# Kernel optimization log

Measured on AMD Instinct MI355X. Metric: run time of the kernel, lower is better.

## Reference

```python
import jax, jax.numpy as jnp
import numpy as np

BATCH = 1024
INPUT_DIM = 4096
HV_DIM = 8192          # == 2**NUM_QUBITS, so encode_classical fully overwrites the state
NUM_QUBITS = 13
QUANTUM_DEPTH = 3


def setup_inputs() -> dict:
    key = jax.random.key(0)
    k1, k2, k3 = jax.random.split(key, 3)
    x = jax.random.normal(k1, (BATCH, INPUT_DIM), dtype=jnp.float32)
    # torch nn.Linear weight layout: [out_features, in_features]
    W = jax.random.normal(k2, (HV_DIM, INPUT_DIM), dtype=jnp.float32)
    quantum_params = jax.random.normal(k3, (QUANTUM_DEPTH, NUM_QUBITS), dtype=jnp.float32)
    return {"x": x, "W": W, "quantum_params": quantum_params}


def reference(x, W, quantum_params):
    # projection: classical_hv = x @ W^T  -> [B, HV_DIM]
    classical = x @ W.T
    # encode_classical: normalize, cast to complex, renormalize (second norm is 1;
    # kept for fidelity with the original code path)
    amps = (classical / jnp.linalg.norm(classical, axis=-1, keepdims=True)).astype(jnp.complex64)
    amps = amps / jnp.linalg.norm(amps, axis=-1, keepdims=True)

    # sequential gate sequence: for depth in range(D): for qubit in range(Q):
    #   amps = amps*cos(a/2) + roll(amps, 1)*sin(a/2)*1j
    # each step uses the updated amplitudes -> lax.scan over the flattened angles
    angles = quantum_params.reshape(-1)  # [D*Q], depth-major matching the loop order

    def step(a, angle):
        c = jnp.cos(angle * 0.5)
        s = jnp.sin(angle * 0.5)
        return a * c + jnp.roll(a, 1, axis=-1) * (s * 1j), None

    amps, _ = jax.lax.scan(step, amps, angles)
    return amps  # [B, 2**NUM_QUBITS] complex64 quantum amplitudes
```

## Files before the change

### kernel.cpp

```cpp
#include <hip/hip_runtime.h>
#include <hip/hip_fp16.h>
#include <math.h>

typedef _Float16 half8 __attribute__((ext_vector_type(8)));
typedef __fp16 fp16x2 __attribute__((ext_vector_type(2)));
typedef float f32x4 __attribute__((ext_vector_type(4)));

#define BATCH 1024
#define IN_DIM 4096
#define HV 8192
#define NTAP 40

#define BM 128
#define BN 128
#define BK 32
#define BKP 36

#define BM2 128
#define BN2 256
#define BK2 64
#define NT2 (IN_DIM / BK2)
#define ASZ (BM2 * BK2)
#define BSZ (BN2 * BK2)
#define TSZ (ASZ + BSZ)

#define GLD16(g, l) __builtin_amdgcn_global_load_lds(                          \
    (const __attribute__((address_space(1))) void*)(g),                        \
    (__attribute__((address_space(3))) void*)(l), 16, 0, 0)

static __device__ __forceinline__ half8 pk8(f32x4 a, f32x4 b) {
    union { fp16x2 p[4]; half8 h; } u;
    u.p[0] = __builtin_amdgcn_cvt_pkrtz(a.x, a.y);
    u.p[1] = __builtin_amdgcn_cvt_pkrtz(a.z, a.w);
    u.p[2] = __builtin_amdgcn_cvt_pkrtz(b.x, b.y);
    u.p[3] = __builtin_amdgcn_cvt_pkrtz(b.z, b.w);
    return u.h;
}

typedef _Float16 half4v __attribute__((ext_vector_type(4)));
__global__ __launch_bounds__(256) void cvt_f32_f16(const float4* __restrict__ src,
                                                   half4v* __restrict__ dst, int n4) {
    int i = blockIdx.x * 256 + threadIdx.x;
    if (i < n4) {
        float4 v = src[i];
        half4v h;
        h.x = (_Float16)v.x; h.y = (_Float16)v.y;
        h.z = (_Float16)v.z; h.w = (_Float16)v.w;
        dst[i] = h;
    }
}

__global__ __launch_bounds__(64) void compute_taps(const float* __restrict__ qp,
                                                   float* __restrict__ taps) {
    const int lane = threadIdx.x;
    float qv = (lane < 39) ? qp[lane] : 0.f;
    float pr = (lane == 0) ? 1.f : 0.f;
    float pim = 0.f;
    for (int t = 0; t < 39; t++) {
        float a = __shfl(qv, t, 64) * 0.5f;
        float c = cosf(a), s = sinf(a);
        float ur = __shfl_up(pr, 1, 64);
        float ui = __shfl_up(pim, 1, 64);
        if (lane == 0) { ur = 0.f; ui = 0.f; }
        float nr = c * pr - s * ui;
        float ni = c * pim + s * ur;
        pr = nr; pim = ni;
    }
    if (lane < NTAP) taps[lane] = pr;
}

__global__ __launch_bounds__(512, 2) void gemm_f16(
        const _Float16* __restrict__ A,
        const _Float16* __restrict__ B,
        float* __restrict__ out,
        long out_n) {
    __shared__ __align__(16) _Float16 lds[3 * TSZ];

    const int tid  = threadIdx.x;
    const int lane = tid & 63;
    const int wave = tid >> 6;
    const int wm = wave & 1;
    const int wn = wave >> 1;
    const int q = lane >> 4, r = lane & 15;
    const int bm = blockIdx.y * BM2;
    const int bn = blockIdx.x * BN2;

    const _Float16* srcA[2];
    int dA[2];
    #pragma unroll
    for (int h = 0; h < 2; h++) {
        const int p = h * 512 + tid;
        const int R = p >> 3, c = (p & 7) ^ (R & 7);
        srcA[h] = A + (size_t)(bm + R) * IN_DIM + c * 8;
        dA[h] = (h * 512 + wave * 64) * 8;
    }
    const _Float16* srcB[4];
    int dB[4];
    #pragma unroll
    for (int h = 0; h < 4; h++) {
        const int p = h * 512 + tid;
        const int R = p >> 3, c = (p & 7) ^ (R & 7);
        srcB[h] = B + (size_t)(bn + R) * IN_DIM + c * 8;
        dB[h] = ASZ + (h * 512 + wave * 64) * 8;
    }

    f32x4 acc[4][4] = {};

#define STAGE(u, k0)  do {                                   \
        _Float16* bp = &lds[(u) * TSZ];                      \
        GLD16(srcA[0] + (k0), bp + dA[0]);                   \
        GLD16(srcA[1] + (k0), bp + dA[1]);                   \
        GLD16(srcB[0] + (k0), bp + dB[0]);                   \
        GLD16(srcB[1] + (k0), bp + dB[1]);                   \
        GLD16(srcB[2] + (k0), bp + dB[2]);                   \
        GLD16(srcB[3] + (k0), bp + dB[3]);                   \
    } while (0)

#define COMPUTE(u)  do {                                                            \
        const _Float16* bp = &lds[(u) * TSZ];                                       \
        half8 af[4][2], bf[4][2];                                                   \
        _Pragma("unroll")                                                           \
        for (int i = 0; i < 4; i++)                                                 \
            _Pragma("unroll")                                                       \
            for (int kk = 0; kk < 2; kk++) {                                        \
                const int R = wm * 64 + i * 16 + r;                                 \
                const int sw = (kk * 4 + q) ^ (r & 7);                              \
                af[i][kk] = *(const half8*)&bp[R * 64 + sw * 8];                    \
            }                                                                       \
        _Pragma("unroll")                                                           \
        for (int j = 0; j < 4; j++)                                                 \
            _Pragma("unroll")                                                       \
            for (int kk = 0; kk < 2; kk++) {                                        \
                const int R = wn * 64 + j * 16 + r;                                 \
                const int sw = (kk * 4 + q) ^ (r & 7);                              \
                bf[j][kk] = *(const half8*)&bp[ASZ + R * 64 + sw * 8];              \
            }                                                                       \
        __builtin_amdgcn_s_setprio(1);                                              \
        _Pragma("unroll")                                                           \
        for (int i = 0; i < 4; i++)                                                 \
            _Pragma("unroll")                                                       \
            for (int j = 0; j < 4; j++)                                             \
                _Pragma("unroll")                                                   \
                for (int kk = 0; kk < 2; kk++)                                      \
                    acc[i][j] = __builtin_amdgcn_mfma_f32_16x16x32_f16(             \
                        af[i][kk], bf[j][kk], acc[i][j], 0, 0, 0);                  \
        __builtin_amdgcn_s_setprio(0);                                              \
    } while (0)

    STAGE(0, 0);
    STAGE(1, BK2);
    int cur = 0;
    for (int t = 0; t < NT2 - 1; ++t) {
        asm volatile("s_waitcnt vmcnt(6)" ::: "memory");
        __builtin_amdgcn_sched_barrier(0);
        __builtin_amdgcn_s_barrier();
        if (t + 2 < NT2) {
            const int nxt = (cur + 2 >= 3) ? cur - 1 : cur + 2;
            STAGE(nxt, (t + 2) * BK2);
        }
        COMPUTE(cur);
        cur = (cur + 1 == 3) ? 0 : cur + 1;
    }
    asm volatile("s_waitcnt vmcnt(0)" ::: "memory");
    __builtin_amdgcn_sched_barrier(0);
    __builtin_amdgcn_s_barrier();
    COMPUTE(cur);
#undef STAGE
#undef COMPUTE

    #pragma unroll
    for (int i = 0; i < 4; i++) {
        const int row = bm + wm * 64 + i * 16 + q * 4;
        #pragma unroll
        for (int j = 0; j < 4; j++) {
            const int col = bn + wn * 64 + j * 16 + r;
            #pragma unroll
            for (int reg = 0; reg < 4; reg++) {
                long idx = (long)(row + reg) * HV + col;
                if (idx < out_n) out[idx] = acc[i][j][reg];
            }
        }
    }
}

__global__ __launch_bounds__(256) void gemm_f32in(
        const float* __restrict__ A, const float* __restrict__ B,
        float* __restrict__ out, long out_n) {
    __shared__ __align__(16) float lgA[BM * BKP];
    __shared__ __align__(16) float lgB[BN * BKP];

    const int tid  = threadIdx.x;
    const int lane = tid & 63;
    const int wave = tid >> 6;
    const int wm = wave & 1, wn = wave >> 1;
    const int q = lane >> 4, r = lane & 15;
    const int bm = blockIdx.y * BM;
    const int bn = blockIdx.x * BN;

    const int rg = lane >> 3;
    const int cg = (lane & 7) * 4;
    const float* gA = A + (size_t)(bm + wave * 32 + rg) * IN_DIM + cg;
    const float* gB = B + (size_t)(bn + wave * 32 + rg) * IN_DIM + cg;
    float* lA = &lgA[(wave * 32 + rg) * BKP + cg];
    float* lB = &lgB[(wave * 32 + rg) * BKP + cg];

    f32x4 acc[4][4] = {};

    for (int k0 = 0; k0 < IN_DIM; k0 += BK) {
        float4 va[4], vb[4];
        #pragma unroll
        for (int i = 0; i < 4; i++) {
            va[i] = *(const float4*)(gA + k0 + (size_t)(8 * i) * IN_DIM);
            vb[i] = *(const float4*)(gB + k0 + (size_t)(8 * i) * IN_DIM);
        }
        __syncthreads();
        #pragma unroll
        for (int i = 0; i < 4; i++) {
            *(float4*)(lA + 8 * i * BKP) = va[i];
            *(float4*)(lB + 8 * i * BKP) = vb[i];
        }
        __syncthreads();

        half8 af[4], bf[4];
        #pragma unroll
        for (int i = 0; i < 4; i++) {
            const float* p = &lgA[(wm * 64 + i * 16 + r) * BKP + q * 8];
            af[i] = pk8(*(const f32x4*)p, *(const f32x4*)(p + 4));
        }
        #pragma unroll
        for (int j = 0; j < 4; j++) {
            const float* p = &lgB[(wn * 64 + j * 16 + r) * BKP + q * 8];
            bf[j] = pk8(*(const f32x4*)p, *(const f32x4*)(p + 4));
        }

        #pragma unroll
        for (int i = 0; i < 4; i++)
            #pragma unroll
            for (int j = 0; j < 4; j++)
                acc[i][j] = __builtin_amdgcn_mfma_f32_16x16x32_f16(af[i], bf[j], acc[i][j], 0, 0, 0);
    }

    #pragma unroll
    for (int i = 0; i < 4; i++) {
        const int row = bm + wm * 64 + i * 16 + q * 4;
        #pragma unroll
        for (int j = 0; j < 4; j++) {
            const int col = bn + wn * 64 + j * 16 + r;
            #pragma unroll
            for (int reg = 0; reg < 4; reg++) {
                long idx = (long)(row + reg) * HV + col;
                if (idx < out_n) out[idx] = acc[i][j][reg];
            }
        }
    }
}

#define SW4(p4) ((p4) ^ (((p4) >> 3) & 7))
__global__ __launch_bounds__(256) void norm_conv(float* __restrict__ out,
                                                 const float* __restrict__ qp,
                                                 const float* __restrict__ taps,
                                                 long out_n) {
    __shared__ __align__(16) float ldsv[40 + HV + 24];
    __shared__ float scr[NTAP];
    __shared__ float red[4];

    const int b = blockIdx.x;
    if ((long)(b + 1) * HV > out_n) return;

    const int tid = threadIdx.x;
    const int lane = tid & 63;
    const int wave = tid >> 6;
    float* rowp = out + (size_t)b * HV;
    const float4* row4 = (const float4*)rowp;
    float4* l4 = (float4*)ldsv;

    float ss = 0.f;
    #pragma unroll
    for (int it = 0; it < 8; it++) {
        int j = it * 256 + tid;
        float4 v = row4[j];
        ss += v.x * v.x + v.y * v.y + v.z * v.z + v.w * v.w;
        l4[SW4(10 + j)] = v;
    }
    if (tid < NTAP) {
        ldsv[(SW4(tid >> 2) << 2) | (tid & 3)] = rowp[HV - NTAP + tid];
    }

    #pragma unroll
    for (int off = 32; off > 0; off >>= 1) ss += __shfl_down(ss, off, 64);
    if (lane == 0) red[wave] = ss;

    if (taps) {
        if (tid < NTAP) scr[tid] = taps[tid];
    } else if (wave == 0) {
        float qv = (lane < 39) ? qp[lane] : 0.f;
        float pr = (lane == 0) ? 1.f : 0.f;
        float pim = 0.f;
        for (int t = 0; t < 39; t++) {
            float a = __shfl(qv, t, 64) * 0.5f;
            float c = cosf(a), s = sinf(a);
            float ur = __shfl_up(pr, 1, 64);
            float ui = __shfl_up(pim, 1, 64);
            if (lane == 0) { ur = 0.f; ui = 0.f; }
            float nr = c * pr - s * ui;
            float ni = c * pim + s * ur;
            pr = nr; pim = ni;
        }
        if (lane < NTAP) scr[lane] = pr;
    }
    __syncthreads();

    const float inv = 1.0f / sqrtf(red[0] + red[1] + red[2] + red[3]);

    float w[72];
    #pragma unroll
    for (int t = 0; t < 18; t++) ((float4*)w)[t] = l4[SW4(8 * tid + t)];

    float4* out4 = (float4*)rowp;
    #pragma unroll
    for (int h = 0; h < 2; h++) {
        float av[16] = {};
        #pragma unroll
        for (int k = 0; k < NTAP; k++) {
            const float c = scr[k];
            #pragma unroll
            for (int o = 0; o < 16; o++) av[o] += c * w[40 + h * 16 + o - k];
        }
        #pragma unroll
        for (int t = 0; t < 4; t++) {
            out4[8 * tid + 4 * h + t] = make_float4(inv * av[4 * t], inv * av[4 * t + 1],
                                                    inv * av[4 * t + 2], inv * av[4 * t + 3]);
        }
    }
}

extern "C" void kernel_launch(void* const* d_in, const int* in_sizes, int n_in,
                              void* d_out, int out_size, void* d_ws, size_t ws_size,
                              hipStream_t stream) {
    const float* x  = (const float*)d_in[0];
    const float* W  = (const float*)d_in[1];
    const float* qp = (const float*)d_in[2];
    float* out = (float*)d_out;
    long out_n = (long)out_size;

    const size_t need = (size_t)BATCH * IN_DIM * 2 + (size_t)HV * IN_DIM * 2;

    if (ws_size >= need) {
        _Float16* xh = (_Float16*)d_ws;
        _Float16* wh = xh + (size_t)BATCH * IN_DIM;
        float* taps = nullptr;
        if (ws_size >= need + 256) {
            taps = (float*)((char*)d_ws + need);
            compute_taps<<<1, 64, 0, stream>>>(qp, taps);
        }
        int n4x = BATCH * IN_DIM / 4;
        int n4w = HV * IN_DIM / 4;
        cvt_f32_f16<<<n4x / 256, 256, 0, stream>>>((const float4*)x, (half4v*)xh, n4x);
        cvt_f32_f16<<<n4w / 256, 256, 0, stream>>>((const float4*)W, (half4v*)wh, n4w);
        dim3 grid2(HV / BN2, BATCH / BM2);
        gemm_f16<<<grid2, 512, 0, stream>>>(xh, wh, out, out_n);
        norm_conv<<<BATCH, 256, 0, stream>>>(out, qp, taps, out_n);
    } else {
        float* taps = nullptr;
        if (ws_size >= 256) {
            taps = (float*)d_ws;
            compute_taps<<<1, 64, 0, stream>>>(qp, taps);
        }
        dim3 grid(HV / BN, BATCH / BM);
        gemm_f32in<<<grid, 256, 0, stream>>>(x, W, out, out_n);
        norm_conv<<<BATCH, 256, 0, stream>>>(out, qp, taps, out_n);
    }
}
```

Measured before the change: 303.5 us.

## Split GEMM k-tile compute into four barrier-separated LDS-read/MFMA phases

Replaces the single per-tile block of LDS reads followed by 32 MFMAs with four phases. Each phase reads a slice of A/B fragments and issues 8 MFMAs, with workgroup barriers between phases so waves interleave LDS traffic with matrix work, similar to the ping-pong scheduling used in hipBLASLt-style kernels. It also lowers the fragment register footprint and moves the vmcnt wait to the end of the tile. The cost is eight extra s_barrier calls per k-step, which may serialise waves and add sync overhead.

```diff
diff --git a/kernel.cpp b/kernel.cpp
--- a/kernel.cpp
+++ b/kernel.cpp
@@ -107,66 +107,90 @@
     f32x4 acc[4][4] = {};
 
 #define STAGE(u, k0)  do {                                   \
-        _Float16* bp = &lds[(u) * TSZ];                      \
-        GLD16(srcA[0] + (k0), bp + dA[0]);                   \
-        GLD16(srcA[1] + (k0), bp + dA[1]);                   \
-        GLD16(srcB[0] + (k0), bp + dB[0]);                   \
-        GLD16(srcB[1] + (k0), bp + dB[1]);                   \
-        GLD16(srcB[2] + (k0), bp + dB[2]);                   \
-        GLD16(srcB[3] + (k0), bp + dB[3]);                   \
+        _Float16* bpS = &lds[(u) * TSZ];                     \
+        GLD16(srcA[0] + (k0), bpS + dA[0]);                  \
+        GLD16(srcA[1] + (k0), bpS + dA[1]);                  \
+        GLD16(srcB[0] + (k0), bpS + dB[0]);                  \
+        GLD16(srcB[1] + (k0), bpS + dB[1]);                  \
+        GLD16(srcB[2] + (k0), bpS + dB[2]);                  \
+        GLD16(srcB[3] + (k0), bpS + dB[3]);                  \
     } while (0)
 
-#define COMPUTE(u)  do {                                                            \
-        const _Float16* bp = &lds[(u) * TSZ];                                       \
-        half8 af[4][2], bf[4][2];                                                   \
-        _Pragma("unroll")                                                           \
-        for (int i = 0; i < 4; i++)                                                 \
-            _Pragma("unroll")                                                       \
-            for (int kk = 0; kk < 2; kk++) {                                        \
-                const int R = wm * 64 + i * 16 + r;                                 \
-                const int sw = (kk * 4 + q) ^ (r & 7);                              \
-                af[i][kk] = *(const half8*)&bp[R * 64 + sw * 8];                    \
-            }                                                                       \
-        _Pragma("unroll")                                                           \
-        for (int j = 0; j < 4; j++)                                                 \
-            _Pragma("unroll")                                                       \
-            for (int kk = 0; kk < 2; kk++) {                                        \
-                const int R = wn * 64 + j * 16 + r;                                 \
-                const int sw = (kk * 4 + q) ^ (r & 7);                              \
-                bf[j][kk] = *(const half8*)&bp[ASZ + R * 64 + sw * 8];              \
-            }                                                                       \
-        __builtin_amdgcn_s_setprio(1);                                              \
-        _Pragma("unroll")                                                           \
-        for (int i = 0; i < 4; i++)                                                 \
-            _Pragma("unroll")                                                       \
-            for (int j = 0; j < 4; j++)                                             \
-                _Pragma("unroll")                                                   \
-                for (int kk = 0; kk < 2; kk++)                                      \
-                    acc[i][j] = __builtin_amdgcn_mfma_f32_16x16x32_f16(             \
-                        af[i][kk], bf[j][kk], acc[i][j], 0, 0, 0);                  \
-        __builtin_amdgcn_s_setprio(0);                                              \
+#define RD_A(dst, kk)  do {                                                        \
+        _Pragma("unroll")                                                          \
+        for (int i = 0; i < 4; i++) {                                              \
+            const int R = wm * 64 + i * 16 + r;                                    \
+            const int sw = ((kk) * 4 + q) ^ (r & 7);                               \
+            dst[i] = *(const half8*)&bp[R * 64 + sw * 8];                          \
+        }                                                                          \
+    } while (0)
+#define RD_B(dst, kk, jh)  do {                                                    \
+        _Pragma("unroll")                                                          \
+        for (int jj = 0; jj < 2; jj++) {                                           \
+            const int R = wn * 64 + ((jh) * 2 + jj) * 16 + r;                      \
+            const int sw = ((kk) * 4 + q) ^ (r & 7);                               \
+            dst[jj] = *(const half8*)&bp[ASZ + R * 64 + sw * 8];                   \
+        }                                                                          \
+    } while (0)
+#define MFMA8(afv, bfv, jh)  do {                                                  \
+        __builtin_amdgcn_s_setprio(1);                                             \
+        _Pragma("unroll")                                                          \
+        for (int i = 0; i < 4; i++)                                                \
+            _Pragma("unroll")                                                      \
+            for (int jj = 0; jj < 2; jj++)                                         \
+                acc[i][(jh) * 2 + jj] = __builtin_amdgcn_mfma_f32_16x16x32_f16(    \
+                    afv[i], bfv[jj], acc[i][(jh) * 2 + jj], 0, 0, 0);              \
+        __builtin_amdgcn_s_setprio(0);                                             \
     } while (0)
 
     STAGE(0, 0);
     STAGE(1, BK2);
+    asm volatile("s_waitcnt vmcnt(6)" ::: "memory");
+    __builtin_amdgcn_sched_barrier(0);
+    __builtin_amdgcn_s_barrier();
+
     int cur = 0;
-    for (int t = 0; t < NT2 - 1; ++t) {
-        asm volatile("s_waitcnt vmcnt(6)" ::: "memory");
-        __builtin_amdgcn_sched_barrier(0);
-        __builtin_amdgcn_s_barrier();
+    for (int t = 0; t < NT2; ++t) {
+        const _Float16* bp = &lds[cur * TSZ];
+        half8 afA[4], afB[4], bf[2];
+
+        RD_A(afA, 0);
+        RD_B(bf, 0, 0);
         if (t + 2 < NT2) {
             const int nxt = (cur + 2 >= 3) ? cur - 1 : cur + 2;
             STAGE(nxt, (t + 2) * BK2);
         }
-        COMPUTE(cur);
+        __builtin_amdgcn_s_barrier();
+        MFMA8(afA, bf, 0);
+        __builtin_amdgcn_s_barrier();
+
+        RD_B(bf, 0, 1);
+        __builtin_amdgcn_s_barrier();
+        MFMA8(afA, bf, 1);
+        __builtin_amdgcn_s_barrier();
+
+        RD_A(afB, 1);
+        RD_B(bf, 1, 0);
+        __builtin_amdgcn_s_barrier();
+        MFMA8(afB, bf, 0);
+        __builtin_amdgcn_s_barrier();
+
+        RD_B(bf, 1, 1);
+        if (t + 1 < NT2) {
+            if (t + 2 < NT2) { asm volatile("s_waitcnt vmcnt(6)" ::: "memory"); }
+            else             { asm volatile("s_waitcnt vmcnt(0)" ::: "memory"); }
+            __builtin_amdgcn_sched_barrier(0);
+        }
+        __builtin_amdgcn_s_barrier();
+        MFMA8(afB, bf, 1);
+        __builtin_amdgcn_s_barrier();
+
         cur = (cur + 1 == 3) ? 0 : cur + 1;
     }
-    asm volatile("s_waitcnt vmcnt(0)" ::: "memory");
-    __builtin_amdgcn_sched_barrier(0);
-    __builtin_amdgcn_s_barrier();
-    COMPUTE(cur);
 #undef STAGE
-#undef COMPUTE
+#undef RD_A
+#undef RD_B
+#undef MFMA8
 
     #pragma unroll
     for (int i = 0; i < 4; i++) {
```

New measurement: 313.2 us. 3.2% more time.
